# Kernel optimization log

Hardware: AMD Instinct MI355X
Metric: run time of the kernel (lower is better)

The kernel has to match this reference:

```python
import jax, jax.numpy as jnp
import numpy as np

V, P, TY, D, H, L, B, T = 30522, 512, 2, 768, 12, 12, 8, 512
DF = 4 * D


def layer_norm(x, g, b, eps=1e-5):
    m = jnp.mean(x, axis=-1, keepdims=True)
    v = jnp.var(x, axis=-1, keepdims=True)
    return (x - m) * jax.lax.rsqrt(v + eps) * g + b


def new_gelu(x):
    c = np.sqrt(2.0 / np.pi).astype(np.float32)
    return 0.5 * x * (1.0 + jnp.tanh(c * (x + 0.044715 * x * x * x)))


def setup_inputs() -> dict:
    key = jax.random.key(0)
    ks = jax.random.split(key, 10)
    s = 0.02
    n = lambda k, shape: (jax.random.normal(k, shape, jnp.float32) * s)
    return dict(
        input_ids=jax.random.randint(ks[0], (B, T), 0, V),
        token_type_ids=jax.random.randint(ks[1], (B, T), 0, TY),
        attention_mask=jnp.ones((B, T), jnp.float32),
        word_emb=n(ks[2], (V, D)),
        pos_emb=n(ks[3], (P, D)),
        type_emb=n(ks[4], (TY, D)),
        emb_ln_g=jnp.ones((D,), jnp.float32), emb_ln_b=jnp.zeros((D,), jnp.float32),
        ln1_g=jnp.ones((L, D), jnp.float32), ln1_b=jnp.zeros((L, D), jnp.float32),
        wqkv=n(ks[5], (L, D, 3 * D)), bqkv=jnp.zeros((L, 3 * D), jnp.float32),
        wproj=n(ks[6], (L, D, D)) / np.sqrt(2 * L).astype(np.float32),
        bproj=jnp.zeros((L, D), jnp.float32),
        ln2_g=jnp.ones((L, D), jnp.float32), ln2_b=jnp.zeros((L, D), jnp.float32),
        wfc=n(ks[7], (L, D, DF)), bfc=jnp.zeros((L, DF), jnp.float32),
        wfc2=n(ks[8], (L, DF, D)) / np.sqrt(2 * L).astype(np.float32),
        bfc2=jnp.zeros((L, D), jnp.float32),
    )


def reference(input_ids, token_type_ids, attention_mask, word_emb, pos_emb, type_emb,
              emb_ln_g, emb_ln_b, ln1_g, ln1_b, wqkv, bqkv, wproj, bproj,
              ln2_g, ln2_b, wfc, bfc, wfc2, bfc2):
    Bx, Tx = input_ids.shape
    hd = D // H
    scale = np.float32(1.0 / np.sqrt(hd))
    # embeddings: word + position + token-type, then LayerNorm (dropout = 0)
    x = word_emb[input_ids] + pos_emb[:Tx][None, :, :] + type_emb[token_type_ids]
    x = layer_norm(x, emb_ln_g, emb_ln_b)
    # additive mask bias, broadcast over heads and query positions: [B,1,1,T]
    mask_bias = (1.0 - attention_mask)[:, None, None, :] * (-10000.0)

    def block(x, p):
        l1g, l1b, wq, bq, wp, bp, l2g, l2b, wf, bf, w2, b2 = p
        h = layer_norm(x, l1g, l1b)
        qkv = h @ wq + bq                                   # [B,T,3D]
        q, k, v = jnp.split(qkv, 3, axis=-1)
        q = q.reshape(Bx, Tx, H, hd).transpose(0, 2, 1, 3)  # [B,H,T,hd]
        k = k.reshape(Bx, Tx, H, hd).transpose(0, 2, 1, 3)
        v = v.reshape(Bx, Tx, H, hd).transpose(0, 2, 1, 3)
        att = jnp.einsum('bhqd,bhkd->bhqk', q, k) * scale + mask_bias
        att = jax.nn.softmax(att, axis=-1)
        y = jnp.einsum('bhqk,bhkd->bhqd', att, v)
        y = y.transpose(0, 2, 1, 3).reshape(Bx, Tx, D)
        x = x + (y @ wp + bp)                               # attn residual
        h2 = layer_norm(x, l2g, l2b)
        h2 = new_gelu(h2 @ wf + bf) @ w2 + b2               # GELU MLP
        return x + h2, None

    x, _ = jax.lax.scan(block, x, (ln1_g, ln1_b, wqkv, bqkv, wproj, bproj,
                                   ln2_g, ln2_b, wfc, bfc, wfc2, bfc2))
    # baseline MLM head: weight tied to word embeddings, no bias
    logits = x @ word_emb.T                                 # [B,T,V]
    return logits
```

## Files before the change

kernel.cpp:

```cpp
#include <hip/hip_runtime.h>
#include <hip/hip_bf16.h>

typedef unsigned short u16;
typedef __attribute__((ext_vector_type(4))) float f32x4;
typedef __attribute__((ext_vector_type(8))) __bf16 bf16x8;

#define DEV static __device__ __forceinline__

DEV float b2f(u16 v) { return __uint_as_float(((unsigned)v) << 16); }

DEV u16 f2b(float f) {
  unsigned u = __float_as_uint(f);
  return (u16)((u + 0x7fffu + ((u >> 16) & 1u)) >> 16);
}

DEV unsigned pk2(float a, float b) {
  return (unsigned)f2b(a) | ((unsigned)f2b(b) << 16);
}

DEV void gload16(const void* g, void* l) {
  __builtin_amdgcn_global_load_lds(
      (__attribute__((address_space(1))) void*)g,
      (__attribute__((address_space(3))) void*)l, 16, 0, 0);
}

DEV float wave_sum(float v) {
  #pragma unroll
  for (int o = 32; o; o >>= 1) v += __shfl_xor(v, o, 64);
  return v;
}

__global__ __launch_bounds__(256)
void embed_ln_k(const int* __restrict__ ids, const int* __restrict__ tts,
                const float* __restrict__ we, const float* __restrict__ pe,
                const float* __restrict__ te, const float* __restrict__ g,
                const float* __restrict__ bb, float* __restrict__ x) {
  const int t = blockIdx.x;
  const int pos = t & 511;
  const int tid = threadIdx.x, lane = tid & 63, w = tid >> 6;
  const int id = ids[t], tt = tts[t];
  __shared__ float red[8];
  float e[3];
  #pragma unroll
  for (int k = 0; k < 3; k++) {
    int d = tid + k * 256;
    e[k] = we[(size_t)id * 768 + d] + pe[(size_t)pos * 768 + d] + te[(size_t)tt * 768 + d];
  }
  float s = wave_sum(e[0] + e[1] + e[2]);
  if (lane == 0) red[w] = s;
  __syncthreads();
  const float mean = (red[0] + red[1] + red[2] + red[3]) * (1.f / 768.f);
  float v2 = 0.f;
  #pragma unroll
  for (int k = 0; k < 3; k++) { float d = e[k] - mean; v2 += d * d; }
  v2 = wave_sum(v2);
  if (lane == 0) red[4 + w] = v2;
  __syncthreads();
  const float var = (red[4] + red[5] + red[6] + red[7]) * (1.f / 768.f);
  const float rstd = rsqrtf(var + 1e-5f);
  #pragma unroll
  for (int k = 0; k < 3; k++) {
    int d = tid + k * 256;
    x[(size_t)t * 768 + d] = (e[k] - mean) * rstd * g[d] + bb[d];
  }
}

__global__ __launch_bounds__(256)
void ln_k(const float* __restrict__ xin, const float* __restrict__ g,
          const float* __restrict__ bb, u16* __restrict__ out) {
  const int lane = threadIdx.x & 63, w = threadIdx.x >> 6;
  const int t = blockIdx.x * 4 + w;
  const float4* x4 = (const float4*)(xin + (size_t)t * 768);
  float4 e[3];
  #pragma unroll
  for (int k = 0; k < 3; k++) e[k] = x4[k * 64 + lane];
  float s = 0.f;
  #pragma unroll
  for (int k = 0; k < 3; k++) s += e[k].x + e[k].y + e[k].z + e[k].w;
  s = wave_sum(s);
  const float mean = s * (1.f / 768.f);
  float v2 = 0.f;
  #pragma unroll
  for (int k = 0; k < 3; k++) {
    float a = e[k].x - mean, b = e[k].y - mean, c = e[k].z - mean, d = e[k].w - mean;
    v2 += a * a + b * b + c * c + d * d;
  }
  v2 = wave_sum(v2);
  const float rstd = rsqrtf(v2 * (1.f / 768.f) + 1e-5f);
  uint2* o2 = (uint2*)(out + (size_t)t * 768);
  #pragma unroll
  for (int k = 0; k < 3; k++) {
    float4 gv = ((const float4*)g)[k * 64 + lane];
    float4 bv = ((const float4*)bb)[k * 64 + lane];
    uint2 o;
    o.x = pk2((e[k].x - mean) * rstd * gv.x + bv.x, (e[k].y - mean) * rstd * gv.y + bv.y);
    o.y = pk2((e[k].z - mean) * rstd * gv.z + bv.z, (e[k].w - mean) * rstd * gv.w + bv.w);
    o2[k * 64 + lane] = o;
  }
}

__global__ __launch_bounds__(256)
void cast_k(const float* __restrict__ xin, u16* __restrict__ out) {
  const int i = blockIdx.x * 256 + threadIdx.x;
  float4 v = ((const float4*)xin)[i];
  uint2 o;
  o.x = pk2(v.x, v.y);
  o.y = pk2(v.z, v.w);
  ((uint2*)out)[i] = o;
}

__global__ __launch_bounds__(256)
void wecast_k(const float* __restrict__ we, u16* __restrict__ out) {
  const int i = blockIdx.x * 256 + threadIdx.x;
  const int row = i / 96, c8 = i % 96;
  uint2 o0 = make_uint2(0u, 0u), o1 = make_uint2(0u, 0u);
  if (row < 30522) {
    const float* src = we + (size_t)row * 768 + c8 * 8;
    float4 a = ((const float4*)src)[0];
    float4 b = ((const float4*)src)[1];
    o0.x = pk2(a.x, a.y); o0.y = pk2(a.z, a.w);
    o1.x = pk2(b.x, b.y); o1.y = pk2(b.z, b.w);
  }
  uint2* dst = (uint2*)(out + (size_t)i * 8);
  dst[0] = o0;
  dst[1] = o1;
}

DEV void tconv_tile(const float* __restrict__ W, u16* __restrict__ Wt,
                    int K, int N, int n0, int k0, int tid, u16 (*t)[65]) {
  const int kl = tid >> 4, nl4 = (tid & 15) * 4;
  #pragma unroll
  for (int i = 0; i < 4; i++) {
    float4 v = *(const float4*)(W + (size_t)(k0 + kl + i * 16) * N + n0 + nl4);
    t[nl4 + 0][kl + i * 16] = f2b(v.x);
    t[nl4 + 1][kl + i * 16] = f2b(v.y);
    t[nl4 + 2][kl + i * 16] = f2b(v.z);
    t[nl4 + 3][kl + i * 16] = f2b(v.w);
  }
  __syncthreads();
  const int nl = tid >> 2, kc = (tid & 3) * 16;
  unsigned wd[8];
  #pragma unroll
  for (int j = 0; j < 8; j++)
    wd[j] = (unsigned)t[nl][kc + 2 * j] | ((unsigned)t[nl][kc + 2 * j + 1] << 16);
  int4* dst = (int4*)(Wt + (size_t)(n0 + nl) * K + k0 + kc);
  dst[0] = make_int4((int)wd[0], (int)wd[1], (int)wd[2], (int)wd[3]);
  dst[1] = make_int4((int)wd[4], (int)wd[5], (int)wd[6], (int)wd[7]);
}

__global__ __launch_bounds__(256)
void tconv_k(const float* __restrict__ W, u16* __restrict__ Wt, int K, int N) {
  __shared__ u16 t[64][65];
  tconv_tile(W, Wt, K, N, blockIdx.x * 64, blockIdx.y * 64, threadIdx.x, t);
}

__global__ __launch_bounds__(256)
void tconv_all_k(const float* __restrict__ wqkv, const float* __restrict__ wprj,
                 const float* __restrict__ wfc, const float* __restrict__ wfc2,
                 u16* __restrict__ wall) {
  __shared__ u16 ts[64][65];
  const int tile = blockIdx.x;
  const int l = tile / 1728, t = tile % 1728;
  u16* base = wall + (size_t)l * 7077888;
  const float* W; u16* Wt; int K, N, loc;
  if (t < 432)       { W = wqkv + (size_t)l * 768 * 2304; Wt = base;           K = 768;  N = 2304; loc = t; }
  else if (t < 576)  { W = wprj + (size_t)l * 768 * 768;  Wt = base + 1769472; K = 768;  N = 768;  loc = t - 432; }
  else if (t < 1152) { W = wfc  + (size_t)l * 768 * 3072; Wt = base + 2359296; K = 768;  N = 3072; loc = t - 576; }
  else               { W = wfc2 + (size_t)l * 3072 * 768; Wt = base + 4718592; K = 3072; N = 768;  loc = t - 1152; }
  const int nbl = N >> 6;
  tconv_tile(W, Wt, K, N, (loc % nbl) * 64, (loc / nbl) * 64, threadIdx.x, ts);
}

template <int EPI>
__global__ __launch_bounds__(256)
void gemm_k(const u16* __restrict__ A, const u16* __restrict__ B,
            const float* __restrict__ bias, const float* __restrict__ resid,
            void* __restrict__ Cptr, int Ndim, int Kdim, int Nblk) {
  __shared__ __align__(16) u16 As[128 * 64];
  __shared__ __align__(16) u16 Bs[128 * 64];
  const int tid = threadIdx.x, lane = tid & 63, w = tid >> 6;
  const int wr = w >> 1, wc = w & 1, fr = lane & 15, fq = lane >> 4;

  const int nwg = gridDim.x, chunk = nwg >> 3;
  const int tile = (blockIdx.x & 7) * chunk + (blockIdx.x >> 3);
  const int nb = tile % Nblk, mb = tile / Nblk;
  const int n0 = nb * 128, m0 = mb * 128;

  f32x4 acc[4][4] = {};
  const int rl = lane >> 3;
  const int sl = ((lane & 7) ^ rl) * 8;

  for (int k0 = 0; k0 < Kdim; k0 += 64) {
    #pragma unroll
    for (int i = 0; i < 4; i++) {
      const int row = i * 32 + w * 8 + rl;
      gload16(A + (size_t)(m0 + row) * Kdim + k0 + sl, As + (i * 32 + w * 8) * 64);
      gload16(B + (size_t)(n0 + row) * Kdim + k0 + sl, Bs + (i * 32 + w * 8) * 64);
    }
    __syncthreads();
    #pragma unroll
    for (int kh = 0; kh < 2; kh++) {
      const int ks = ((kh * 4 + fq) ^ (fr & 7)) * 8;
      bf16x8 af[4], bfv[4];
      #pragma unroll
      for (int m = 0; m < 4; m++)
        af[m] = *(const bf16x8*)(&As[(wr * 64 + m * 16 + fr) * 64 + ks]);
      #pragma unroll
      for (int n = 0; n < 4; n++)
        bfv[n] = *(const bf16x8*)(&Bs[(wc * 64 + n * 16 + fr) * 64 + ks]);
      #pragma unroll
      for (int m = 0; m < 4; m++)
        #pragma unroll
        for (int n = 0; n < 4; n++)
          acc[m][n] = __builtin_amdgcn_mfma_f32_16x16x32_bf16(af[m], bfv[n], acc[m][n], 0, 0, 0);
    }
    __syncthreads();
  }

  #pragma unroll
  for (int m = 0; m < 4; m++) {
    const int row = m0 + wr * 64 + m * 16 + fq * 4;
    #pragma unroll
    for (int n = 0; n < 4; n++) {
      const int col = n0 + wc * 64 + n * 16 + fr;
      const float bv = (bias != nullptr) ? bias[col] : 0.f;
      #pragma unroll
      for (int r = 0; r < 4; r++) {
        float v = acc[m][n][r] + bv;
        const size_t idx = (size_t)(row + r) * Ndim + col;
        if (EPI == 0) {
          ((u16*)Cptr)[idx] = f2b(v);
        } else if (EPI == 1) {
          float t = v;
          float gl = 0.5f * t * (1.f + tanhf(0.7978845608f * (t + 0.044715f * t * t * t)));
          ((u16*)Cptr)[idx] = f2b(gl);
        } else if (EPI == 2) {
          ((float*)Cptr)[idx] = resid[idx] + v;
        }
      }
    }
  }
}

template <int EPI>
__global__ __launch_bounds__(256)
void gemm64_k(const u16* __restrict__ A, const u16* __restrict__ B,
              const float* __restrict__ bias, const float* __restrict__ resid,
              void* __restrict__ Cptr, int Ndim, int Kdim, int Nblk) {
  __shared__ __align__(16) u16 As[64 * 64];
  __shared__ __align__(16) u16 Bs[64 * 64];
  const int tid = threadIdx.x, lane = tid & 63, w = tid >> 6;
  const int wr = w >> 1, wc = w & 1, fr = lane & 15, fq = lane >> 4;

  const int nwg = gridDim.x, chunk = nwg >> 3;
  const int tile = (blockIdx.x & 7) * chunk + (blockIdx.x >> 3);
  const int nb = tile % Nblk, mb = tile / Nblk;
  const int n0 = nb * 64, m0 = mb * 64;

  f32x4 acc[2][2] = {};
  const int rl = lane >> 3;
  const int sl = ((lane & 7) ^ rl) * 8;

  for (int k0 = 0; k0 < Kdim; k0 += 64) {
    #pragma unroll
    for (int i = 0; i < 2; i++) {
      const int row = i * 32 + w * 8 + rl;
      gload16(A + (size_t)(m0 + row) * Kdim + k0 + sl, As + (i * 32 + w * 8) * 64);
      gload16(B + (size_t)(n0 + row) * Kdim + k0 + sl, Bs + (i * 32 + w * 8) * 64);
    }
    __syncthreads();
    #pragma unroll
    for (int kh = 0; kh < 2; kh++) {
      const int ks = ((kh * 4 + fq) ^ (fr & 7)) * 8;
      bf16x8 af[2], bfv[2];
      #pragma unroll
      for (int m = 0; m < 2; m++)
        af[m] = *(const bf16x8*)(&As[(wr * 32 + m * 16 + fr) * 64 + ks]);
      #pragma unroll
      for (int n = 0; n < 2; n++)
        bfv[n] = *(const bf16x8*)(&Bs[(wc * 32 + n * 16 + fr) * 64 + ks]);
      #pragma unroll
      for (int m = 0; m < 2; m++)
        #pragma unroll
        for (int n = 0; n < 2; n++)
          acc[m][n] = __builtin_amdgcn_mfma_f32_16x16x32_bf16(af[m], bfv[n], acc[m][n], 0, 0, 0);
    }
    __syncthreads();
  }

  #pragma unroll
  for (int m = 0; m < 2; m++) {
    const int row = m0 + wr * 32 + m * 16 + fq * 4;
    #pragma unroll
    for (int n = 0; n < 2; n++) {
      const int col = n0 + wc * 32 + n * 16 + fr;
      const float bv = (bias != nullptr) ? bias[col] : 0.f;
      #pragma unroll
      for (int r = 0; r < 4; r++) {
        float v = acc[m][n][r] + bv;
        const size_t idx = (size_t)(row + r) * Ndim + col;
        if (EPI == 0) {
          ((u16*)Cptr)[idx] = f2b(v);
        } else if (EPI == 1) {
          float t = v;
          float gl = 0.5f * t * (1.f + tanhf(0.7978845608f * (t + 0.044715f * t * t * t)));
          ((u16*)Cptr)[idx] = f2b(gl);
        } else if (EPI == 2) {
          ((float*)Cptr)[idx] = resid[idx] + v;
        }
      }
    }
  }
}

__global__ __launch_bounds__(256)
void gemm256_k(const u16* __restrict__ A, const u16* __restrict__ B,
               float* __restrict__ Cptr, int Ndim, int Kdim, int Nblk) {
  __shared__ __align__(16) u16 As[2][256 * 32];
  __shared__ __align__(16) u16 Bs[2][128 * 32];
  const int tid = threadIdx.x, lane = tid & 63, w = tid >> 6;
  const int fr = lane & 15, fq = lane >> 4;

  const int nwg = gridDim.x, chunk = nwg >> 3;
  const int tile = (blockIdx.x & 7) * chunk + (blockIdx.x >> 3);
  const int nb = tile % Nblk, mb = tile / Nblk;
  const int n0 = nb * 128, m0 = mb * 256;

  f32x4 acc[4][8] = {};
  const int r0l = lane >> 2;
  const int sl = ((lane & 3) ^ (r0l & 3)) * 8;

  #define STAGE256(k0, buf)                                                     \
    {                                                                           \
      _Pragma("unroll")                                                         \
      for (int i = 0; i < 4; i++) {                                             \
        const int st = i * 4 + w;                                               \
        gload16(A + (size_t)(m0 + st * 16 + r0l) * Kdim + (k0) + sl,            \
                &As[buf][st * 512]);                                            \
      }                                                                         \
      _Pragma("unroll")                                                         \
      for (int i = 0; i < 2; i++) {                                             \
        const int st = i * 4 + w;                                               \
        gload16(B + (size_t)(n0 + st * 16 + r0l) * Kdim + (k0) + sl,            \
                &Bs[buf][st * 512]);                                            \
      }                                                                         \
    }

  STAGE256(0, 0);
  __syncthreads();
  int buf = 0;

  for (int k0 = 0; k0 < Kdim; k0 += 32) {
    if (k0 + 32 < Kdim) STAGE256(k0 + 32, buf ^ 1);
    const int ks = (fq ^ (fr & 3)) * 8;
    bf16x8 af[4], bfv[8];
    #pragma unroll
    for (int m = 0; m < 4; m++)
      af[m] = *(const bf16x8*)(&As[buf][(w * 64 + m * 16 + fr) * 32 + ks]);
    #pragma unroll
    for (int n = 0; n < 8; n++)
      bfv[n] = *(const bf16x8*)(&Bs[buf][(n * 16 + fr) * 32 + ks]);
    #pragma unroll
    for (int m = 0; m < 4; m++)
      #pragma unroll
      for (int n = 0; n < 8; n++)
        acc[m][n] = __builtin_amdgcn_mfma_f32_16x16x32_bf16(af[m], bfv[n], acc[m][n], 0, 0, 0);
    __syncthreads();
    buf ^= 1;
  }
  #undef STAGE256

  #pragma unroll
  for (int m = 0; m < 4; m++) {
    const int row = m0 + w * 64 + m * 16 + fq * 4;
    #pragma unroll
    for (int n = 0; n < 8; n++) {
      const int col = n0 + n * 16 + fr;
      if (col >= Ndim) continue;
      #pragma unroll
      for (int r = 0; r < 4; r++)
        Cptr[(size_t)(row + r) * Ndim + col] = acc[m][n][r];
    }
  }
}

__global__ __launch_bounds__(256)
void attn_mfma_k(const u16* __restrict__ qkv, const float* __restrict__ amask,
                 u16* __restrict__ y) {
  __shared__ __align__(16) u16 Ks[2][64 * 64];
  __shared__ __align__(16) u16 Vt[2][64 * 64];
  __shared__ __align__(16) u16 Ps[4][16 * 64];
  __shared__ float bias_lds[512];
  const int tid = threadIdx.x, lane = tid & 63, w = tid >> 6;
  const int bh = blockIdx.y, b = bh / 12, hh = bh % 12;
  const int q0 = blockIdx.x * 64;
  const u16* qb = qkv + (size_t)(b * 512) * 2304 + hh * 64;
  const u16* kb = qb + 768;
  const u16* vb = qb + 1536;
  const int fr = lane & 15, fq = lane >> 4;

  bias_lds[tid] = (1.0f - amask[b * 512 + tid]) * -10000.0f;
  bias_lds[tid + 256] = (1.0f - amask[b * 512 + tid + 256]) * -10000.0f;

  bf16x8 af[2];
  {
    const u16* qrow = qb + (size_t)(q0 + w * 16 + fr) * 2304;
    af[0] = *(const bf16x8*)(qrow + fq * 8);
    af[1] = *(const bf16x8*)(qrow + 32 + fq * 8);
  }

  auto stageK = [&](int kt, int nb) {
    const int r0 = lane >> 3, dc = lane & 7, s = dc ^ r0;
    #pragma unroll
    for (int p = 0; p < 2; p++) {
      const int i = w * 2 + p;
      gload16(kb + (size_t)(kt * 64 + i * 8 + r0) * 2304 + s * 8,
              (void*)&Ks[nb][i * 512]);
    }
  };
  auto stageV = [&](int kt, int nb) {
    #pragma unroll
    for (int p = 0; p < 2; p++) {
      const int dc = w * 2 + p;
      int4 vd = *(const int4*)(vb + (size_t)(kt * 64 + lane) * 2304 + dc * 8);
      union { int4 v; u16 e[8]; } u; u.v = vd;
      #pragma unroll
      for (int ii = 0; ii < 8; ii++)
        Vt[nb][(dc * 8 + ii) * 64 + (lane ^ (ii << 3))] = u.e[ii];
    }
  };

  f32x4 O[4];
  #pragma unroll
  for (int nd = 0; nd < 4; nd++) O[nd] = f32x4{0.f, 0.f, 0.f, 0.f};
  float run_m = -3.0e38f, run_l = 0.f;

  stageK(0, 0); stageV(0, 0);
  __syncthreads();
  int cur = 0;

  for (int kt = 0; kt < 8; kt++) {
    if (kt < 7) { stageK(kt + 1, cur ^ 1); stageV(kt + 1, cur ^ 1); }

    f32x4 sacc[4];
    #pragma unroll
    for (int n = 0; n < 4; n++) sacc[n] = f32x4{0.f, 0.f, 0.f, 0.f};
    __builtin_amdgcn_s_setprio(1);
    #pragma unroll
    for (int n = 0; n < 4; n++)
      #pragma unroll
      for (int kh = 0; kh < 2; kh++) {
        bf16x8 kf = *(const bf16x8*)(&Ks[cur][(n * 16 + fr) * 64 + ((kh * 4 + fq) ^ (fr & 7)) * 8]);
        sacc[n] = __builtin_amdgcn_mfma_f32_16x16x32_bf16(kf, af[kh], sacc[n], 0, 0, 0);
      }
    __builtin_amdgcn_s_setprio(0);

    float s[4][4];
    float vm = -3.0e38f;
    #pragma unroll
    for (int n = 0; n < 4; n++) {
      float4 b4 = *(const float4*)(&bias_lds[kt * 64 + n * 16 + fq * 4]);
      s[n][0] = sacc[n][0] * 0.125f + b4.x;
      s[n][1] = sacc[n][1] * 0.125f + b4.y;
      s[n][2] = sacc[n][2] * 0.125f + b4.z;
      s[n][3] = sacc[n][3] * 0.125f + b4.w;
      vm = fmaxf(vm, fmaxf(fmaxf(s[n][0], s[n][1]), fmaxf(s[n][2], s[n][3])));
    }
    vm = fmaxf(vm, __shfl_xor(vm, 16, 64));
    vm = fmaxf(vm, __shfl_xor(vm, 32, 64));
    const float nm = fmaxf(run_m, vm);
    const float al = __expf(run_m - nm);
    run_m = nm;
    float p[4][4], ts = 0.f;
    #pragma unroll
    for (int n = 0; n < 4; n++)
      #pragma unroll
      for (int r = 0; r < 4; r++) { p[n][r] = __expf(s[n][r] - nm); ts += p[n][r]; }
    ts += __shfl_xor(ts, 16, 64);
    ts += __shfl_xor(ts, 32, 64);
    run_l = run_l * al + ts;
    #pragma unroll
    for (int nd = 0; nd < 4; nd++) O[nd] *= al;

    #pragma unroll
    for (int n = 0; n < 4; n++) {
      uint2 dw;
      dw.x = pk2(p[n][0], p[n][1]);
      dw.y = pk2(p[n][2], p[n][3]);
      const int slot = (2 * n + (fq >> 1)) ^ (fr & 7);
      *(uint2*)((char*)&Ps[w][0] + fr * 128 + slot * 16 + (fq & 1) * 8) = dw;
    }
    asm volatile("s_waitcnt lgkmcnt(0)" ::: "memory");
    __builtin_amdgcn_sched_barrier(0);

    bf16x8 pb[2];
    #pragma unroll
    for (int kh = 0; kh < 2; kh++)
      pb[kh] = *(const bf16x8*)((char*)&Ps[w][0] + fr * 128 + (((kh * 4 + fq) ^ (fr & 7)) * 16));
    __builtin_amdgcn_s_setprio(1);
    #pragma unroll
    for (int nd = 0; nd < 4; nd++) {
      bf16x8 vf0 = *(const bf16x8*)(&Vt[cur][(nd * 16 + fr) * 64 + ((0 + fq) ^ (fr & 7)) * 8]);
      bf16x8 vf1 = *(const bf16x8*)(&Vt[cur][(nd * 16 + fr) * 64 + ((4 + fq) ^ (fr & 7)) * 8]);
      O[nd] = __builtin_amdgcn_mfma_f32_16x16x32_bf16(vf0, pb[0], O[nd], 0, 0, 0);
      O[nd] = __builtin_amdgcn_mfma_f32_16x16x32_bf16(vf1, pb[1], O[nd], 0, 0, 0);
    }
    __builtin_amdgcn_s_setprio(0);
    __syncthreads();
    cur ^= 1;
  }

  const float inv = 1.0f / run_l;
  u16* yrow = y + (size_t)(b * 512 + q0 + w * 16 + fr) * 768 + hh * 64;
  #pragma unroll
  for (int nd = 0; nd < 4; nd++) {
    uint2 o;
    o.x = pk2(O[nd][0] * inv, O[nd][1] * inv);
    o.y = pk2(O[nd][2] * inv, O[nd][3] * inv);
    *(uint2*)(yrow + nd * 16 + fq * 4) = o;
  }
}

extern "C" void kernel_launch(void* const* d_in, const int* in_sizes, int n_in,
                              void* d_out, int out_size, void* d_ws, size_t ws_size,
                              hipStream_t stream) {
  (void)in_sizes; (void)n_in; (void)out_size;
  const int*   ids  = (const int*)d_in[0];
  const int*   tts  = (const int*)d_in[1];
  const float* am   = (const float*)d_in[2];
  const float* we   = (const float*)d_in[3];
  const float* pe   = (const float*)d_in[4];
  const float* te   = (const float*)d_in[5];
  const float* eg   = (const float*)d_in[6];
  const float* eb   = (const float*)d_in[7];
  const float* l1g  = (const float*)d_in[8];
  const float* l1b  = (const float*)d_in[9];
  const float* wqkv = (const float*)d_in[10];
  const float* bqkv = (const float*)d_in[11];
  const float* wprj = (const float*)d_in[12];
  const float* bprj = (const float*)d_in[13];
  const float* l2g  = (const float*)d_in[14];
  const float* l2b  = (const float*)d_in[15];
  const float* wfc  = (const float*)d_in[16];
  const float* bfc  = (const float*)d_in[17];
  const float* wfc2 = (const float*)d_in[18];
  const float* bfc2 = (const float*)d_in[19];

  char* ws = (char*)d_ws;
  float* x   = (float*)ws;
  u16*  h    = (u16*)(ws + 12582912);
  u16*  qkv  = (u16*)(ws + 18874368);
  u16*  y    = (u16*)(ws + 37748736);
  u16*  fc   = (u16*)(ws + 18874368);
  u16*  we_b = (u16*)(ws + 44040192);
  u16*  wall = (u16*)(ws + 91029504);
  const bool upfront = ws_size >= 260898816ull;
  u16* wqkv_f = (u16*)(ws + 91029504);
  u16* wprj_f = wqkv_f + 1769472;
  u16* wfc_f  = wqkv_f + 2359296;
  u16* wfc2_f = wqkv_f + 4718592;

  wecast_k<<<11472, 256, 0, stream>>>(we, we_b);
  embed_ln_k<<<4096, 256, 0, stream>>>(ids, tts, we, pe, te, eg, eb, x);
  if (upfront)
    tconv_all_k<<<20736, 256, 0, stream>>>(wqkv, wprj, wfc, wfc2, wall);

  for (int l = 0; l < 12; l++) {
    u16 *wq_b, *wp_b, *wf_b, *w2_b;
    if (upfront) {
      u16* base = wall + (size_t)l * 7077888;
      wq_b = base; wp_b = base + 1769472; wf_b = base + 2359296; w2_b = base + 4718592;
    } else {
      tconv_k<<<dim3(36, 12), 256, 0, stream>>>(wqkv + (size_t)l * 768 * 2304, wqkv_f, 768, 2304);
      tconv_k<<<dim3(12, 12), 256, 0, stream>>>(wprj + (size_t)l * 768 * 768,  wprj_f, 768, 768);
      tconv_k<<<dim3(48, 12), 256, 0, stream>>>(wfc  + (size_t)l * 768 * 3072, wfc_f,  768, 3072);
      tconv_k<<<dim3(12, 48), 256, 0, stream>>>(wfc2 + (size_t)l * 3072 * 768, wfc2_f, 3072, 768);
      wq_b = wqkv_f; wp_b = wprj_f; wf_b = wfc_f; w2_b = wfc2_f;
    }

    ln_k<<<1024, 256, 0, stream>>>(x, l1g + l * 768, l1b + l * 768, h);
    gemm_k<0><<<576, 256, 0, stream>>>(
        h, wq_b, bqkv + l * 2304, nullptr, qkv, 2304, 768, 18);
    attn_mfma_k<<<dim3(8, 96), 256, 0, stream>>>(qkv, am, y);
    gemm64_k<2><<<768, 256, 0, stream>>>(
        y, wp_b, bprj + l * 768, x, x, 768, 768, 12);
    ln_k<<<1024, 256, 0, stream>>>(x, l2g + l * 768, l2b + l * 768, h);
    gemm_k<1><<<768, 256, 0, stream>>>(
        h, wf_b, bfc + l * 3072, nullptr, fc, 3072, 768, 24);
    gemm64_k<2><<<768, 256, 0, stream>>>(
        fc, w2_b, bfc2 + l * 768, x, x, 768, 3072, 12);
  }

  cast_k<<<3072, 256, 0, stream>>>(x, h);
  gemm256_k<<<3824, 256, 0, stream>>>(
      h, we_b, (float*)d_out, 30522, 768, 239);
}
```

Measured before the change: 2.298 ms.

## Double-buffer LDS in 128/64 GEMMs with BK=32 and revise swizzle pattern

Converts the single-buffered BK=64 gemm_k and gemm64_k loops into double-buffered BK=32 pipelines that prefetch the next K slice while MFMAs run on the current one, matching the gemm256 structure. The LDS XOR swizzle is changed to key on (row>>1)&3 instead of row&3, in all three GEMMs, to cut bank conflicts on the 64-byte rows. This removes one barrier per iteration and exposes load/compute overlap. In exchange it halves the MFMA work per barrier and doubles the loop trip count.

```diff
diff --git a/kernel.cpp b/kernel.cpp
--- a/kernel.cpp
+++ b/kernel.cpp
@@ -176,8 +176,8 @@
 void gemm_k(const u16* __restrict__ A, const u16* __restrict__ B,
             const float* __restrict__ bias, const float* __restrict__ resid,
             void* __restrict__ Cptr, int Ndim, int Kdim, int Nblk) {
-  __shared__ __align__(16) u16 As[128 * 64];
-  __shared__ __align__(16) u16 Bs[128 * 64];
+  __shared__ __align__(16) u16 As[2][128 * 32];
+  __shared__ __align__(16) u16 Bs[2][128 * 32];
   const int tid = threadIdx.x, lane = tid & 63, w = tid >> 6;
   const int wr = w >> 1, wc = w & 1, fr = lane & 15, fq = lane >> 4;
 
@@ -187,35 +187,42 @@
   const int n0 = nb * 128, m0 = mb * 128;
 
   f32x4 acc[4][4] = {};
-  const int rl = lane >> 3;
-  const int sl = ((lane & 7) ^ rl) * 8;
-
-  for (int k0 = 0; k0 < Kdim; k0 += 64) {
-    #pragma unroll
-    for (int i = 0; i < 4; i++) {
-      const int row = i * 32 + w * 8 + rl;
-      gload16(A + (size_t)(m0 + row) * Kdim + k0 + sl, As + (i * 32 + w * 8) * 64);
-      gload16(B + (size_t)(n0 + row) * Kdim + k0 + sl, Bs + (i * 32 + w * 8) * 64);
-    }
+  const int rq = lane >> 2;
+  const int sl = ((lane & 3) ^ ((lane >> 3) & 3)) * 8;
+
+  #define GSTAGE(k0, buf)                                                 \
+    { _Pragma("unroll")                                                   \
+      for (int p = 0; p < 2; p++) {                                       \
+        const int st = w * 2 + p;                                         \
+        gload16(A + (size_t)(m0 + st * 16 + rq) * Kdim + (k0) + sl,       \
+                &As[buf][st * 512]);                                      \
+        gload16(B + (size_t)(n0 + st * 16 + rq) * Kdim + (k0) + sl,       \
+                &Bs[buf][st * 512]);                                      \
+      } }
+
+  GSTAGE(0, 0);
+  __syncthreads();
+  int buf = 0;
+
+  for (int k0 = 0; k0 < Kdim; k0 += 32) {
+    if (k0 + 32 < Kdim) GSTAGE(k0 + 32, buf ^ 1);
+    const int ks = (fq ^ ((fr >> 1) & 3)) * 8;
+    bf16x8 af[4], bfv[4];
+    #pragma unroll
+    for (int m = 0; m < 4; m++)
+      af[m] = *(const bf16x8*)(&As[buf][(wr * 64 + m * 16 + fr) * 32 + ks]);
+    #pragma unroll
+    for (int n = 0; n < 4; n++)
+      bfv[n] = *(const bf16x8*)(&Bs[buf][(wc * 64 + n * 16 + fr) * 32 + ks]);
+    #pragma unroll
+    for (int m = 0; m < 4; m++)
+      #pragma unroll
+      for (int n = 0; n < 4; n++)
+        acc[m][n] = __builtin_amdgcn_mfma_f32_16x16x32_bf16(af[m], bfv[n], acc[m][n], 0, 0, 0);
     __syncthreads();
-    #pragma unroll
-    for (int kh = 0; kh < 2; kh++) {
-      const int ks = ((kh * 4 + fq) ^ (fr & 7)) * 8;
-      bf16x8 af[4], bfv[4];
-      #pragma unroll
-      for (int m = 0; m < 4; m++)
-        af[m] = *(const bf16x8*)(&As[(wr * 64 + m * 16 + fr) * 64 + ks]);
-      #pragma unroll
-      for (int n = 0; n < 4; n++)
-        bfv[n] = *(const bf16x8*)(&Bs[(wc * 64 + n * 16 + fr) * 64 + ks]);
-      #pragma unroll
-      for (int m = 0; m < 4; m++)
-        #pragma unroll
-        for (int n = 0; n < 4; n++)
-          acc[m][n] = __builtin_amdgcn_mfma_f32_16x16x32_bf16(af[m], bfv[n], acc[m][n], 0, 0, 0);
-    }
-    __syncthreads();
-  }
+    buf ^= 1;
+  }
+  #undef GSTAGE
 
   #pragma unroll
   for (int m = 0; m < 4; m++) {
@@ -247,8 +254,8 @@
 void gemm64_k(const u16* __restrict__ A, const u16* __restrict__ B,
               const float* __restrict__ bias, const float* __restrict__ resid,
               void* __restrict__ Cptr, int Ndim, int Kdim, int Nblk) {
-  __shared__ __align__(16) u16 As[64 * 64];
-  __shared__ __align__(16) u16 Bs[64 * 64];
+  __shared__ __align__(16) u16 As[2][64 * 32];
+  __shared__ __align__(16) u16 Bs[2][64 * 32];
   const int tid = threadIdx.x, lane = tid & 63, w = tid >> 6;
   const int wr = w >> 1, wc = w & 1, fr = lane & 15, fq = lane >> 4;
 
@@ -258,35 +265,40 @@
   const int n0 = nb * 64, m0 = mb * 64;
 
   f32x4 acc[2][2] = {};
-  const int rl = lane >> 3;
-  const int sl = ((lane & 7) ^ rl) * 8;
-
-  for (int k0 = 0; k0 < Kdim; k0 += 64) {
-    #pragma unroll
-    for (int i = 0; i < 2; i++) {
-      const int row = i * 32 + w * 8 + rl;
-      gload16(A + (size_t)(m0 + row) * Kdim + k0 + sl, As + (i * 32 + w * 8) * 64);
-      gload16(B + (size_t)(n0 + row) * Kdim + k0 + sl, Bs + (i * 32 + w * 8) * 64);
-    }
+  const int rq = lane >> 2;
+  const int sl = ((lane & 3) ^ ((lane >> 3) & 3)) * 8;
+
+  #define GSTAGE64(k0, buf)                                              \
+    {                                                                     \
+      gload16(A + (size_t)(m0 + w * 16 + rq) * Kdim + (k0) + sl,          \
+              &As[buf][w * 512]);                                         \
+      gload16(B + (size_t)(n0 + w * 16 + rq) * Kdim + (k0) + sl,          \
+              &Bs[buf][w * 512]);                                         \
+    }
+
+  GSTAGE64(0, 0);
+  __syncthreads();
+  int buf = 0;
+
+  for (int k0 = 0; k0 < Kdim; k0 += 32) {
+    if (k0 + 32 < Kdim) GSTAGE64(k0 + 32, buf ^ 1);
+    const int ks = (fq ^ ((fr >> 1) & 3)) * 8;
+    bf16x8 af[2], bfv[2];
+    #pragma unroll
+    for (int m = 0; m < 2; m++)
+      af[m] = *(const bf16x8*)(&As[buf][(wr * 32 + m * 16 + fr) * 32 + ks]);
+    #pragma unroll
+    for (int n = 0; n < 2; n++)
+      bfv[n] = *(const bf16x8*)(&Bs[buf][(wc * 32 + n * 16 + fr) * 32 + ks]);
+    #pragma unroll
+    for (int m = 0; m < 2; m++)
+      #pragma unroll
+      for (int n = 0; n < 2; n++)
+        acc[m][n] = __builtin_amdgcn_mfma_f32_16x16x32_bf16(af[m], bfv[n], acc[m][n], 0, 0, 0);
     __syncthreads();
-    #pragma unroll
-    for (int kh = 0; kh < 2; kh++) {
-      const int ks = ((kh * 4 + fq) ^ (fr & 7)) * 8;
-      bf16x8 af[2], bfv[2];
-      #pragma unroll
-      for (int m = 0; m < 2; m++)
-        af[m] = *(const bf16x8*)(&As[(wr * 32 + m * 16 + fr) * 64 + ks]);
-      #pragma unroll
-      for (int n = 0; n < 2; n++)
-        bfv[n] = *(const bf16x8*)(&Bs[(wc * 32 + n * 16 + fr) * 64 + ks]);
-      #pragma unroll
-      for (int m = 0; m < 2; m++)
-        #pragma unroll
-        for (int n = 0; n < 2; n++)
-          acc[m][n] = __builtin_amdgcn_mfma_f32_16x16x32_bf16(af[m], bfv[n], acc[m][n], 0, 0, 0);
-    }
-    __syncthreads();
-  }
+    buf ^= 1;
+  }
+  #undef GSTAGE64
 
   #pragma unroll
   for (int m = 0; m < 2; m++) {
@@ -327,21 +339,21 @@
   const int n0 = nb * 128, m0 = mb * 256;
 
   f32x4 acc[4][8] = {};
-  const int r0l = lane >> 2;
-  const int sl = ((lane & 3) ^ (r0l & 3)) * 8;
+  const int rq = lane >> 2;
+  const int sl = ((lane & 3) ^ ((lane >> 3) & 3)) * 8;
 
   #define STAGE256(k0, buf)                                                     \
     {                                                                           \
       _Pragma("unroll")                                                         \
       for (int i = 0; i < 4; i++) {                                             \
         const int st = i * 4 + w;                                               \
-        gload16(A + (size_t)(m0 + st * 16 + r0l) * Kdim + (k0) + sl,            \
+        gload16(A + (size_t)(m0 + st * 16 + rq) * Kdim + (k0) + sl,             \
                 &As[buf][st * 512]);                                            \
       }                                                                         \
       _Pragma("unroll")                                                         \
       for (int i = 0; i < 2; i++) {                                             \
         const int st = i * 4 + w;                                               \
-        gload16(B + (size_t)(n0 + st * 16 + r0l) * Kdim + (k0) + sl,            \
+        gload16(B + (size_t)(n0 + st * 16 + rq) * Kdim + (k0) + sl,             \
                 &Bs[buf][st * 512]);                                            \
       }                                                                         \
     }
@@ -352,7 +364,7 @@
 
   for (int k0 = 0; k0 < Kdim; k0 += 32) {
     if (k0 + 32 < Kdim) STAGE256(k0 + 32, buf ^ 1);
-    const int ks = (fq ^ (fr & 3)) * 8;
+    const int ks = (fq ^ ((fr >> 1) & 3)) * 8;
     bf16x8 af[4], bfv[8];
     #pragma unroll
     for (int m = 0; m < 4; m++)
```

New measurement: 2.549 ms. 10.9% more time.
